# Performance work log

Hardware: AMD Instinct MI355X
Metric: run time of the kernel (lower is better)

Reference implementation:

```python
import jax, jax.numpy as jnp
import numpy as np

D_MODEL = 1024
NUM_HEADS = 16
D_K = D_MODEL // NUM_HEADS  # 64
THETA = 10000.0


def setup_inputs() -> dict:
    key = jax.random.key(0)
    k_x, k_q, k_k, k_v, k_o = jax.random.split(key, 5)
    B, S = 2, 2048
    std = (2.0 / (D_MODEL + D_MODEL)) ** 0.5
    x = jax.random.normal(k_x, (B, S, D_MODEL), dtype=jnp.float32)
    Wq = std * jax.random.truncated_normal(k_q, -3.0, 3.0, (D_MODEL, D_MODEL), dtype=jnp.float32)
    Wk = std * jax.random.truncated_normal(k_k, -3.0, 3.0, (D_MODEL, D_MODEL), dtype=jnp.float32)
    Wv = std * jax.random.truncated_normal(k_v, -3.0, 3.0, (D_MODEL, D_MODEL), dtype=jnp.float32)
    Wo = std * jax.random.truncated_normal(k_o, -3.0, 3.0, (D_MODEL, D_MODEL), dtype=jnp.float32)
    return {"x": x, "Wq": Wq, "Wk": Wk, "Wv": Wv, "Wo": Wo}


def _apply_rope(t, cos, sin):
    # t: [B, H, S, d_k]; cos/sin: [S, d_k//2] broadcast over B, H
    tr = t.reshape(*t.shape[:-1], D_K // 2, 2)
    t1, t2 = tr[..., 0], tr[..., 1]
    r1 = t1 * cos - t2 * sin
    r2 = t1 * sin + t2 * cos
    return jnp.stack([r1, r2], axis=-1).reshape(t.shape)


def reference(x, Wq, Wk, Wv, Wo):
    B, S, D = x.shape
    H, dk = NUM_HEADS, D_K
    # projections (no bias): y = x @ W.T
    Q = (x @ Wq.T).reshape(B, S, H, dk).transpose(0, 2, 1, 3)  # [B,H,S,dk]
    K = (x @ Wk.T).reshape(B, S, H, dk).transpose(0, 2, 1, 3)
    V = (x @ Wv.T).reshape(B, S, H, dk).transpose(0, 2, 1, 3)
    # RoPE angles for positions 0..S-1
    pos = jnp.arange(S, dtype=jnp.float32)[:, None]            # [S,1]
    freqs = 1.0 / (THETA ** (jnp.arange(0, dk, 2, dtype=jnp.float32) / dk))  # [dk/2]
    angles = pos * freqs[None, :]                              # [S, dk/2]
    cos, sin = jnp.cos(angles), jnp.sin(angles)
    Q = _apply_rope(Q, cos, sin)
    K = _apply_rope(K, cos, sin)
    # causal scaled dot-product attention
    scores = jnp.einsum("bhqd,bhkd->bhqk", Q, K) / jnp.sqrt(jnp.float32(dk))
    causal = jnp.tril(jnp.ones((S, S), dtype=bool))
    scores = jnp.where(causal, scores, -jnp.inf)
    probs = jax.nn.softmax(scores, axis=-1)
    attn = jnp.einsum("bhqk,bhkd->bhqd", probs, V)             # [B,H,S,dk]
    attn = attn.transpose(0, 2, 1, 3).reshape(B, S, H * dk)
    return attn @ Wo.T
```

## Files before the change

### kernel.cpp

```cpp
#include <hip/hip_runtime.h>
#include <hip/hip_bf16.h>

typedef __bf16 bf16;
typedef __bf16 bf16x8 __attribute__((ext_vector_type(8)));
typedef float f32x4 __attribute__((ext_vector_type(4)));

#define MFMA16(A, B, C) __builtin_amdgcn_mfma_f32_16x16x32_bf16((A), (B), (C), 0, 0, 0)

static __device__ __forceinline__ void gload16(const bf16* g, bf16* l) {
    __builtin_amdgcn_global_load_lds((const __attribute__((address_space(1))) void*)g,
                                     (__attribute__((address_space(3))) void*)l, 16, 0, 0);
}

__global__ void detect_kernel(const void* w, int* flag) {
    float v = (float)((const bf16*)w)[threadIdx.x];
    unsigned long long bad = __ballot(!(fabsf(v) < 1.0f));
    if (threadIdx.x == 0) *flag = bad ? 1 : 0;
}

__global__ __launch_bounds__(256) void convert_all(const void* x, const void* w0,
                                                   const void* w1, const void* w2,
                                                   const void* w3, bf16* xb, bf16* b0,
                                                   bf16* b1, bf16* b2, bf16* b3,
                                                   const int* flagp) {
    if (*flagp == 0) return;
    int id = (blockIdx.x * 256 + threadIdx.x) * 4;
    const int XN = 1 << 22;
    const float* src;
    bf16* dst;
    int off;
    if (id < XN) {
        src = (const float*)x; dst = xb; off = id;
    } else {
        int r = id - XN;
        int wi = r >> 20;
        off = r & ((1 << 20) - 1);
        src = (const float*)(wi == 0 ? w0 : wi == 1 ? w1 : wi == 2 ? w2 : w3);
        dst = (wi == 0 ? b0 : wi == 1 ? b1 : wi == 2 ? b2 : b3);
    }
    float4 v = *(const float4*)(src + off);
    bf16 o[4] = {(bf16)v.x, (bf16)v.y, (bf16)v.z, (bf16)v.w};
    *(uint2*)(dst + off) = *(uint2*)o;
}

__global__ __launch_bounds__(256) void zero_out(float* acc32, float* dout,
                                                const int* flagp) {
    int i = (blockIdx.x * 256 + threadIdx.x) * 4;
    float4 z = {0.f, 0.f, 0.f, 0.f};
    *(float4*)(acc32 + i) = z;
    if (*flagp) *(float4*)(dout + i) = z;
}

__global__ __launch_bounds__(256) void cast_out(const float* acc32, bf16* dout,
                                                const int* flagp) {
    if (*flagp) return;
    int i = (blockIdx.x * 256 + threadIdx.x) * 4;
    float4 v = *(const float4*)(acc32 + i);
    bf16 o[4] = {(bf16)v.x, (bf16)v.y, (bf16)v.z, (bf16)v.w};
    *(uint2*)(dout + i) = *(uint2*)o;
}

template <int MODE>
__global__ __launch_bounds__(128, 3) void gemm_nt(const void* rawA, const bf16* convA,
                                                  const void* rW0, const bf16* cW0,
                                                  const void* rW1, const bf16* cW1,
                                                  const void* rW2, const bf16* cW2,
                                                  bf16* Qo, bf16* Ko, bf16* Vt,
                                                  void* Cout, float* accp,
                                                  const int* flagp) {
    const int K = 1024;
    __shared__ __attribute__((aligned(16))) bf16 lsA[2][128 * 32];
    __shared__ __attribute__((aligned(16))) bf16 lsB[2][64 * 32];
    const int flag = *flagp;
    const bf16* A = flag ? convA : (const bf16*)rawA;
    int tensor, n0, m0, ks;
    const bf16* W;
    if (MODE == 0) {
        tensor = blockIdx.x >> 4;
        n0 = (blockIdx.x & 15) * 64;
        m0 = blockIdx.y * 128;
        ks = 0;
        W = tensor == 0 ? (flag ? cW0 : (const bf16*)rW0)
          : tensor == 1 ? (flag ? cW1 : (const bf16*)rW1)
                        : (flag ? cW2 : (const bf16*)rW2);
    } else {
        const int bid = blockIdx.x;
        ks = bid & 1;
        const int slot = bid >> 1;
        m0 = (slot & 31) * 128;
        n0 = (slot >> 5) * 64;
        tensor = 0;
        W = flag ? cW0 : (const bf16*)rW0;
    }
    const int t = threadIdx.x;
    const int w = t >> 6, lane = t & 63;
    const int llo = lane & 15, quad = lane >> 4;
    const int sel = (llo >> 1) & 3;

    f32x4 acc[4][4] = {};

    auto stage = [&](int k0, int buf) {
#pragma unroll
        for (int j = 0; j < 4; ++j) {
            int c = j * 128 + t;
            int row = c >> 2, pos = c & 3;
            int g = pos ^ ((row >> 1) & 3);
            gload16(A + (size_t)(m0 + row) * K + k0 + g * 8, &lsA[buf][c * 8]);
        }
#pragma unroll
        for (int j = 0; j < 2; ++j) {
            int c = j * 128 + t;
            int row = c >> 2, pos = c & 3;
            int g = pos ^ ((row >> 1) & 3);
            gload16(W + (size_t)(n0 + row) * K + k0 + g * 8, &lsB[buf][c * 8]);
        }
    };

    auto compute = [&](int buf) {
        bf16x8 a[4], bb[4];
#pragma unroll
        for (int mi = 0; mi < 4; ++mi) {
            int r = w * 64 + mi * 16 + llo;
            a[mi] = *(const bf16x8*)&lsA[buf][r * 32 + ((quad ^ sel) * 8)];
        }
#pragma unroll
        for (int ni = 0; ni < 4; ++ni) {
            int r = ni * 16 + llo;
            bb[ni] = *(const bf16x8*)&lsB[buf][r * 32 + ((quad ^ sel) * 8)];
        }
#pragma unroll
        for (int mi = 0; mi < 4; ++mi)
#pragma unroll
            for (int ni = 0; ni < 4; ++ni)
                acc[mi][ni] = MFMA16(a[mi], bb[ni], acc[mi][ni]);
    };

    const int kbase = (MODE == 1) ? ks * 512 : 0;
    const int NIT = (MODE == 1) ? 16 : 32;

    stage(kbase, 0);
    for (int it = 0; it < NIT; it += 2) {
        __syncthreads();
        stage(kbase + (it + 1) * 32, 1);
        compute(0);
        __syncthreads();
        if (it + 2 < NIT) stage(kbase + (it + 2) * 32, 0);
        compute(1);
    }

#pragma unroll
    for (int mi = 0; mi < 4; ++mi)
#pragma unroll
        for (int ni = 0; ni < 4; ++ni)
#pragma unroll
            for (int r = 0; r < 4; ++r) {
                int row = m0 + w * 64 + mi * 16 + quad * 4 + r;
                int col = n0 + ni * 16 + llo;
                float v = acc[mi][ni][r];
                if (MODE == 1) {
                    float* dst = flag ? (float*)Cout : accp;
                    atomicAdd(&dst[(size_t)row * 1024 + col], v);
                } else if (tensor == 2) {
                    int b = row >> 11, s = row & 2047;
                    Vt[((size_t)b * 1024 + col) * 2048 + s] = (bf16)v;
                } else {
                    int d = col & 63, s = row & 2047;
                    float partner = __shfl_xor(v, 1);
                    float freq = exp2f((float)(d >> 1) * -0.4152410118609203f);
                    float rev = (float)s * freq * 0.15915494309189535f;
                    rev -= floorf(rev);
                    float sn = __builtin_amdgcn_sinf(rev);
                    float cs = __builtin_amdgcn_cosf(rev);
                    float outv = v * cs + partner * sn * ((d & 1) ? 1.0f : -1.0f);
                    bf16* dst = (tensor == 0) ? Qo : Ko;
                    dst[(size_t)row * 1024 + col] = (bf16)outv;
                }
            }
}

__global__ __launch_bounds__(256, 3) void attn_kernel(const bf16* __restrict__ Q,
                                                      const bf16* __restrict__ Kr,
                                                      const bf16* __restrict__ Vt,
                                                      bf16* __restrict__ O,
                                                      bf16* __restrict__ Opart,
                                                      float* __restrict__ lws) {
    __shared__ __attribute__((aligned(16))) bf16 lsK[2][64 * 64];
    __shared__ __attribute__((aligned(16))) bf16 lsV[2][64 * 64];
    __shared__ __attribute__((aligned(16))) bf16 lsP[4][32 * 64];
    const int blk = blockIdx.x;
    int ib, bh, s, tt0, tt1;
    bool split;
    if (blk < 512) {
        split = true;
        s = blk >> 8;
        int c = blk & 255;
        ib = 15 - (c >> 5);
        bh = c & 31;
        tt0 = s ? (ib + 1) : 0;
        tt1 = s ? (2 * ib + 1) : ib;
    } else {
        split = false;
        s = 0;
        int c = blk - 512;
        ib = c >> 5;
        bh = c & 31;
        tt0 = 0;
        tt1 = 2 * ib + 1;
    }
    const int b = bh >> 4, h = bh & 15;
    const int t = threadIdx.x, w = t >> 6, lane = t & 63;
    const int llo = lane & 15, quad = lane >> 4;
    const int q0w = ib * 128 + w * 32;

    bf16x8 aQ[2][2];
#pragma unroll
    for (int qi = 0; qi < 2; ++qi) {
        const size_t qb =
            ((size_t)(b * 2048 + q0w + qi * 16 + llo)) * 1024 + h * 64 + quad * 8;
        aQ[qi][0] = *(const bf16x8*)&Q[qb];
        aQ[qi][1] = *(const bf16x8*)&Q[qb + 32];
    }

    f32x4 o[2][4] = {};
    float lpart[2] = {0.f, 0.f};
    const float SC = 0.18033688011112042f;
    const int qlane0 = q0w + llo;

    const int srow8 = lane >> 3;
    const int sc = (lane & 7) ^ srow8;

    auto stage = [&](int tt, int buf) {
        const int kv0 = tt * 64;
#pragma unroll
        for (int jj = 0; jj < 2; ++jj) {
            int seg = w + jj * 4;
            int rowk = seg * 8 + srow8;
            gload16(&Kr[((size_t)(b * 2048 + kv0 + rowk)) * 1024 + h * 64 + sc * 8],
                    &lsK[buf][seg * 512 + lane * 8]);
            gload16(&Vt[((size_t)(b * 1024 + h * 64 + rowk)) * 2048 + kv0 + sc * 8],
                    &lsV[buf][seg * 512 + lane * 8]);
        }
    };

    stage(tt0, 0);

    for (int tt = tt0; tt <= tt1; ++tt) {
        const int cur = (tt - tt0) & 1;
        const int kv0 = tt * 64;
        __syncthreads();
        if (tt + 1 <= tt1) stage(tt + 1, cur ^ 1);

        if (kv0 <= q0w + 31) {
            bf16x8 kf[4][2];
#pragma unroll
            for (int half = 0; half < 4; ++half) {
                int rk = half * 16 + llo;
                kf[half][0] = *(const bf16x8*)&lsK[cur][rk * 64 + ((quad ^ (rk & 7)) * 8)];
                kf[half][1] =
                    *(const bf16x8*)&lsK[cur][rk * 64 + (((quad + 4) ^ (rk & 7)) * 8)];
            }
            bf16x8 vf[2][4];
#pragma unroll
            for (int kc = 0; kc < 2; ++kc)
#pragma unroll
                for (int g = 0; g < 4; ++g) {
                    int rv = g * 16 + llo;
                    int cg = kc * 4 + quad;
                    vf[kc][g] =
                        *(const bf16x8*)&lsV[cur][rv * 64 + ((cg ^ (rv & 7)) * 8)];
                }

            const bool need_mask = (kv0 + 63 >= q0w);
#pragma unroll
            for (int qi = 0; qi < 2; ++qi) {
                const int q = qlane0 + qi * 16;
                const int prow = qi * 16 + llo;
#pragma unroll
                for (int half = 0; half < 4; ++half) {
                    f32x4 z = {};
                    z = MFMA16(kf[half][0], aQ[qi][0], z);
                    z = MFMA16(kf[half][1], aQ[qi][1], z);
                    union { bf16 hh[4]; uint2 uu; } pk;
                    if (need_mask) {
                        int kvb = kv0 + half * 16 + quad * 4;
#pragma unroll
                        for (int r = 0; r < 4; ++r) {
                            float e = (kvb + r <= q) ? z[r] * SC : -INFINITY;
                            float p = __builtin_amdgcn_exp2f(e);
                            lpart[qi] += p;
                            pk.hh[r] = (bf16)p;
                        }
                    } else {
#pragma unroll
                        for (int r = 0; r < 4; ++r) {
                            float p = __builtin_amdgcn_exp2f(z[r] * SC);
                            lpart[qi] += p;
                            pk.hh[r] = (bf16)p;
                        }
                    }
                    int cw = 2 * half + (quad >> 1);
                    *(uint2*)&lsP[w][prow * 64 + ((cw ^ (llo & 7)) * 8) + (quad & 1) * 4] =
                        pk.uu;
                }
            }
            __builtin_amdgcn_wave_barrier();
#pragma unroll
            for (int qi = 0; qi < 2; ++qi) {
                const int prow = qi * 16 + llo;
#pragma unroll
                for (int kc = 0; kc < 2; ++kc) {
                    int cr = 4 * kc + quad;
                    bf16x8 aP =
                        *(const bf16x8*)&lsP[w][prow * 64 + ((cr ^ (llo & 7)) * 8)];
#pragma unroll
                    for (int g = 0; g < 4; ++g) o[qi][g] = MFMA16(aP, vf[kc][g], o[qi][g]);
                }
            }
            __builtin_amdgcn_wave_barrier();
        }
    }

    float lfull[2];
#pragma unroll
    for (int qi = 0; qi < 2; ++qi) {
        float l = lpart[qi];
        l += __shfl_xor(l, 16);
        l += __shfl_xor(l, 32);
        lfull[qi] = l;
    }

    if (split) {
        const int slotw = ((ib - 8) * 32 + bh) * 2 + s;
        bf16* op = Opart + (size_t)slotw * 8192;
#pragma unroll
        for (int qi = 0; qi < 2; ++qi) {
#pragma unroll
            for (int r = 0; r < 4; ++r) {
                int row_in = w * 32 + qi * 16 + quad * 4 + r;
#pragma unroll
                for (int g = 0; g < 4; ++g)
                    op[row_in * 64 + g * 16 + llo] = (bf16)o[qi][g][r];
            }
            if (quad == 0) lws[slotw * 128 + w * 32 + qi * 16 + llo] = lfull[qi];
        }
    } else {
#pragma unroll
        for (int qi = 0; qi < 2; ++qi)
#pragma unroll
            for (int r = 0; r < 4; ++r) {
                float l = __shfl(lfull[qi], (lane & 48) | (quad * 4 + r));
                float inv = 1.f / l;
                int q = q0w + qi * 16 + quad * 4 + r;
                size_t ob = ((size_t)(b * 2048 + q)) * 1024 + h * 64;
#pragma unroll
                for (int g = 0; g < 4; ++g)
                    O[ob + g * 16 + llo] = (bf16)(o[qi][g][r] * inv);
            }
    }
}

__global__ __launch_bounds__(256) void combine_kernel(const bf16* __restrict__ Opart,
                                                      const float* __restrict__ lws,
                                                      bf16* __restrict__ AO) {
    int id = blockIdx.x * 256 + threadIdx.x;
    int d = id & 63;
    int h = (id >> 6) & 15;
    int qoff = (id >> 10) & 1023;
    int b = id >> 20;
    int ib8 = qoff >> 7;
    int q_in = qoff & 127;
    int slot = (ib8 * 32 + (b * 16 + h)) * 2;
    size_t base = (size_t)slot * 8192 + q_in * 64 + d;
    float o0 = (float)Opart[base];
    float o1 = (float)Opart[base + 8192];
    float l = lws[slot * 128 + q_in] + lws[(slot + 1) * 128 + q_in];
    int q = 1024 + qoff;
    AO[((size_t)(b * 2048 + q)) * 1024 + h * 64 + d] = (bf16)((o0 + o1) / l);
}

extern "C" void kernel_launch(void* const* d_in, const int* in_sizes, int n_in,
                              void* d_out, int out_size, void* d_ws, size_t ws_size,
                              hipStream_t stream) {
    const size_t TN = (size_t)4096 * 1024;

    int* flag = (int*)d_ws;
    bf16* Q = (bf16*)((char*)d_ws + 256);
    bf16* Kb = Q + TN;
    bf16* Vt = Kb + TN;
    bf16* xb = Vt + TN;
    bf16* Wb0 = xb + TN;
    bf16* Wb1 = Wb0 + TN / 4;
    bf16* Wb2 = Wb1 + TN / 4;
    bf16* Wb3 = Wb2 + TN / 4;
    bf16* AO = Q;
    bf16* Opart = xb;
    float* lws = (float*)Wb0;
    float* acc32 = (float*)Kb;

    detect_kernel<<<1, 64, 0, stream>>>(d_in[1], flag);
    convert_all<<<8192, 256, 0, stream>>>(d_in[0], d_in[1], d_in[2], d_in[3], d_in[4],
                                          xb, Wb0, Wb1, Wb2, Wb3, flag);

    gemm_nt<0><<<dim3(48, 32), 128, 0, stream>>>(d_in[0], xb, d_in[1], Wb0, d_in[2],
                                                 Wb1, d_in[3], Wb2, Q, Kb, Vt, nullptr,
                                                 nullptr, flag);

    attn_kernel<<<768, 256, 0, stream>>>(Q, Kb, Vt, AO, Opart, lws);
    combine_kernel<<<8192, 256, 0, stream>>>(Opart, lws, AO);

    zero_out<<<4096, 256, 0, stream>>>(acc32, (float*)d_out, flag);
    gemm_nt<1><<<1024, 128, 0, stream>>>(AO, AO, d_in[4], Wb3, nullptr, nullptr,
                                         nullptr, nullptr, nullptr, nullptr, nullptr,
                                         d_out, acc32, flag);
    cast_out<<<4096, 256, 0, stream>>>(acc32, (bf16*)d_out, flag);
}
```

Before: 224.3 us.

## Enlarge GEMM tiles to 128x128 with 4 waves and replace atomic split-K with partial buffers

The projection and output GEMMs now use 256-thread blocks computing 128x128 tiles, where each of four waves owns a 64x64 quadrant. This doubles the data reuse per staged A/B tile and halves the grid size. The output projection's split-K no longer zero-fills and atomically accumulates. Each K-half writes its own fp32 partial buffer, and a single reduce kernel sums them and writes the output in fp32 or bf16. That drops the zero_out and cast_out launches and the atomic traffic, at the cost of fewer blocks for occupancy and an extra partial buffer read.

```diff
diff --git a/kernel.cpp b/kernel.cpp
--- a/kernel.cpp
+++ b/kernel.cpp
@@ -43,41 +43,24 @@
     *(uint2*)(dst + off) = *(uint2*)o;
 }
 
-__global__ __launch_bounds__(256) void zero_out(float* acc32, float* dout,
-                                                const int* flagp) {
-    int i = (blockIdx.x * 256 + threadIdx.x) * 4;
-    float4 z = {0.f, 0.f, 0.f, 0.f};
-    *(float4*)(acc32 + i) = z;
-    if (*flagp) *(float4*)(dout + i) = z;
-}
-
-__global__ __launch_bounds__(256) void cast_out(const float* acc32, bf16* dout,
-                                                const int* flagp) {
-    if (*flagp) return;
-    int i = (blockIdx.x * 256 + threadIdx.x) * 4;
-    float4 v = *(const float4*)(acc32 + i);
-    bf16 o[4] = {(bf16)v.x, (bf16)v.y, (bf16)v.z, (bf16)v.w};
-    *(uint2*)(dout + i) = *(uint2*)o;
-}
-
 template <int MODE>
-__global__ __launch_bounds__(128, 3) void gemm_nt(const void* rawA, const bf16* convA,
+__global__ __launch_bounds__(256, 3) void gemm_nt(const void* rawA, const bf16* convA,
                                                   const void* rW0, const bf16* cW0,
                                                   const void* rW1, const bf16* cW1,
                                                   const void* rW2, const bf16* cW2,
                                                   bf16* Qo, bf16* Ko, bf16* Vt,
-                                                  void* Cout, float* accp,
+                                                  float* p0, float* p1,
                                                   const int* flagp) {
     const int K = 1024;
     __shared__ __attribute__((aligned(16))) bf16 lsA[2][128 * 32];
-    __shared__ __attribute__((aligned(16))) bf16 lsB[2][64 * 32];
+    __shared__ __attribute__((aligned(16))) bf16 lsB[2][128 * 32];
     const int flag = *flagp;
     const bf16* A = flag ? convA : (const bf16*)rawA;
     int tensor, n0, m0, ks;
     const bf16* W;
     if (MODE == 0) {
-        tensor = blockIdx.x >> 4;
-        n0 = (blockIdx.x & 15) * 64;
+        tensor = blockIdx.x >> 3;
+        n0 = (blockIdx.x & 7) * 128;
         m0 = blockIdx.y * 128;
         ks = 0;
         W = tensor == 0 ? (flag ? cW0 : (const bf16*)rW0)
@@ -88,12 +71,13 @@
         ks = bid & 1;
         const int slot = bid >> 1;
         m0 = (slot & 31) * 128;
-        n0 = (slot >> 5) * 64;
+        n0 = (slot >> 5) * 128;
         tensor = 0;
         W = flag ? cW0 : (const bf16*)rW0;
     }
     const int t = threadIdx.x;
     const int w = t >> 6, lane = t & 63;
+    const int wr = w >> 1, wc = w & 1;
     const int llo = lane & 15, quad = lane >> 4;
     const int sel = (llo >> 1) & 3;
 
@@ -101,15 +85,15 @@
 
     auto stage = [&](int k0, int buf) {
 #pragma unroll
-        for (int j = 0; j < 4; ++j) {
-            int c = j * 128 + t;
+        for (int j = 0; j < 2; ++j) {
+            int c = j * 256 + t;
             int row = c >> 2, pos = c & 3;
             int g = pos ^ ((row >> 1) & 3);
             gload16(A + (size_t)(m0 + row) * K + k0 + g * 8, &lsA[buf][c * 8]);
         }
 #pragma unroll
         for (int j = 0; j < 2; ++j) {
-            int c = j * 128 + t;
+            int c = j * 256 + t;
             int row = c >> 2, pos = c & 3;
             int g = pos ^ ((row >> 1) & 3);
             gload16(W + (size_t)(n0 + row) * K + k0 + g * 8, &lsB[buf][c * 8]);
@@ -120,12 +104,12 @@
         bf16x8 a[4], bb[4];
 #pragma unroll
         for (int mi = 0; mi < 4; ++mi) {
-            int r = w * 64 + mi * 16 + llo;
+            int r = wr * 64 + mi * 16 + llo;
             a[mi] = *(const bf16x8*)&lsA[buf][r * 32 + ((quad ^ sel) * 8)];
         }
 #pragma unroll
         for (int ni = 0; ni < 4; ++ni) {
-            int r = ni * 16 + llo;
+            int r = wc * 64 + ni * 16 + llo;
             bb[ni] = *(const bf16x8*)&lsB[buf][r * 32 + ((quad ^ sel) * 8)];
         }
 #pragma unroll
@@ -154,12 +138,12 @@
         for (int ni = 0; ni < 4; ++ni)
 #pragma unroll
             for (int r = 0; r < 4; ++r) {
-                int row = m0 + w * 64 + mi * 16 + quad * 4 + r;
-                int col = n0 + ni * 16 + llo;
+                int row = m0 + wr * 64 + mi * 16 + quad * 4 + r;
+                int col = n0 + wc * 64 + ni * 16 + llo;
                 float v = acc[mi][ni][r];
                 if (MODE == 1) {
-                    float* dst = flag ? (float*)Cout : accp;
-                    atomicAdd(&dst[(size_t)row * 1024 + col], v);
+                    float* dst = ks ? p1 : p0;
+                    dst[(size_t)row * 1024 + col] = v;
                 } else if (tensor == 2) {
                     int b = row >> 11, s = row & 2047;
                     Vt[((size_t)b * 1024 + col) * 2048 + s] = (bf16)v;
@@ -176,6 +160,20 @@
                     dst[(size_t)row * 1024 + col] = (bf16)outv;
                 }
             }
+}
+
+__global__ __launch_bounds__(256) void reduce_out(const float* p0, const float* p1,
+                                                  void* dout, const int* flagp) {
+    int i = (blockIdx.x * 256 + threadIdx.x) * 4;
+    float4 a = *(const float4*)(p0 + i);
+    float4 b = *(const float4*)(p1 + i);
+    float4 s = {a.x + b.x, a.y + b.y, a.z + b.z, a.w + b.w};
+    if (*flagp) {
+        *(float4*)((float*)dout + i) = s;
+    } else {
+        bf16 o[4] = {(bf16)s.x, (bf16)s.y, (bf16)s.z, (bf16)s.w};
+        *(uint2*)((bf16*)dout + i) = *(uint2*)o;
+    }
 }
 
 __global__ __launch_bounds__(256, 3) void attn_kernel(const bf16* __restrict__ Q,
@@ -395,22 +393,22 @@
     bf16* AO = Q;
     bf16* Opart = xb;
     float* lws = (float*)Wb0;
-    float* acc32 = (float*)Kb;
+    float* p0 = (float*)Kb;
+    float* p1 = (float*)xb;
 
     detect_kernel<<<1, 64, 0, stream>>>(d_in[1], flag);
     convert_all<<<8192, 256, 0, stream>>>(d_in[0], d_in[1], d_in[2], d_in[3], d_in[4],
                                           xb, Wb0, Wb1, Wb2, Wb3, flag);
 
-    gemm_nt<0><<<dim3(48, 32), 128, 0, stream>>>(d_in[0], xb, d_in[1], Wb0, d_in[2],
+    gemm_nt<0><<<dim3(24, 32), 256, 0, stream>>>(d_in[0], xb, d_in[1], Wb0, d_in[2],
                                                  Wb1, d_in[3], Wb2, Q, Kb, Vt, nullptr,
                                                  nullptr, flag);
 
     attn_kernel<<<768, 256, 0, stream>>>(Q, Kb, Vt, AO, Opart, lws);
     combine_kernel<<<8192, 256, 0, stream>>>(Opart, lws, AO);
 
-    zero_out<<<4096, 256, 0, stream>>>(acc32, (float*)d_out, flag);
-    gemm_nt<1><<<1024, 128, 0, stream>>>(AO, AO, d_in[4], Wb3, nullptr, nullptr,
-                                         nullptr, nullptr, nullptr, nullptr, nullptr,
-                                         d_out, acc32, flag);
-    cast_out<<<4096, 256, 0, stream>>>(acc32, (bf16*)d_out, flag);
-}
+    gemm_nt<1><<<512, 256, 0, stream>>>(AO, AO, d_in[4], Wb3, nullptr, nullptr,
+                                        nullptr, nullptr, nullptr, nullptr, nullptr,
+                                        p0, p1, flag);
+    reduce_out<<<4096, 256, 0, stream>>>(p0, p1, d_out, flag);
+}
```

After: 192.3 us. -14.3%, faster.
